# Performance work log

Measured on AMD Instinct MI355X. Metric: run time of the kernel, lower is better.

The kernel has to match this reference:

```python
import jax, jax.numpy as jnp
import numpy as np

NUM_CLASSES = 20
NUM_ANCHORS = 3
STRIDES = (8, 16, 32)
FMP = (320, 160, 80)
TOPK = 100
CONF_THRESH = 0.01
NMS_THRESH = 0.5
ANCHOR_SIZE = np.array([[12, 16], [19, 36], [40, 28], [36, 75], [76, 55], [72, 146],
                        [142, 110], [192, 243], [459, 401]], dtype=np.float32).reshape(3, NUM_ANCHORS, 2)


def make_anchors(level):
    h = w = FMP[level]
    ys, xs = jnp.meshgrid(jnp.arange(h, dtype=jnp.float32), jnp.arange(w, dtype=jnp.float32), indexing='ij')
    xy = jnp.stack([xs, ys], axis=-1).reshape(-1, 1, 2) + 0.5            # [HW,1,2] grid centers
    xy = jnp.broadcast_to(xy, (h * w, NUM_ANCHORS, 2))
    wh = jnp.broadcast_to(jnp.asarray(ANCHOR_SIZE[level]), (h * w, NUM_ANCHORS, 2))
    return jnp.concatenate([xy, wh], axis=-1).reshape(-1, 4)             # [HW*A, 4]


def level_topk(obj, cls, reg, level):
    C = NUM_CLASSES
    # [1, ch, H, W] -> [H*W*A, ch_per_anchor], matching permute(1,2,0).view(-1, .)
    obj = obj[0].transpose(1, 2, 0).reshape(-1, 1)
    cls = cls[0].transpose(1, 2, 0).reshape(-1, C)
    reg = reg[0].transpose(1, 2, 0).reshape(-1, 4)
    anchors = make_anchors(level)
    # decode: ctr = (sigmoid(txy)*3 - 1.5 + grid) * stride ; wh = exp(twh) * anchor_wh
    ctr = (jax.nn.sigmoid(reg[:, :2]) * 3.0 - 1.5 + anchors[:, :2]) * STRIDES[level]
    wh = jnp.exp(reg[:, 2:]) * anchors[:, 2:]
    boxes = jnp.concatenate([ctr - 0.5 * wh, ctr + 0.5 * wh], axis=-1)   # [N, 4] xyxy
    scores = (jax.nn.sigmoid(obj) * jax.nn.sigmoid(cls)).reshape(-1)     # [N*C]
    top_s, top_i = jax.lax.top_k(scores, TOPK)
    anchor_idx = top_i // C
    labels = top_i % C
    return top_s, labels, boxes[anchor_idx], top_s > CONF_THRESH


def nms_fixed(boxes, scores, labels, valid):
    # class-aware greedy NMS on a fixed candidate set; suppressed entries get score 0 / keep False
    K = scores.shape[0]
    order = jnp.argsort(-scores)
    b, s, l, v = boxes[order], scores[order], labels[order], valid[order]
    areas = (b[:, 2] - b[:, 0]) * (b[:, 3] - b[:, 1])
    xx1 = jnp.maximum(b[:, None, 0], b[None, :, 0])
    yy1 = jnp.maximum(b[:, None, 1], b[None, :, 1])
    xx2 = jnp.minimum(b[:, None, 2], b[None, :, 2])
    yy2 = jnp.minimum(b[:, None, 3], b[None, :, 3])
    inter = jnp.maximum(1e-10, xx2 - xx1) * jnp.maximum(1e-10, yy2 - yy1)
    iou = inter / (areas[:, None] + areas[None, :] - inter)
    sup_mat = (iou > NMS_THRESH) & (l[:, None] == l[None, :])            # per-class suppression
    idx = jnp.arange(K)

    def body(i, state):
        suppressed, keep = state
        is_kept = jnp.logical_and(jnp.logical_not(suppressed[i]), v[i])
        keep = keep.at[i].set(is_kept)
        suppressed = suppressed | (is_kept & sup_mat[i] & (idx > i))
        return suppressed, keep

    _, keep = jax.lax.fori_loop(0, K, body, (jnp.zeros(K, bool), jnp.zeros(K, bool)))
    return b, s * keep.astype(s.dtype), l, keep


def setup_inputs() -> dict:
    key = jax.random.key(0)
    ks = jax.random.split(key, 9)
    shapes = {
        'obj0': (1, NUM_ANCHORS, 320, 320), 'cls0': (1, NUM_ANCHORS * NUM_CLASSES, 320, 320), 'reg0': (1, NUM_ANCHORS * 4, 320, 320),
        'obj1': (1, NUM_ANCHORS, 160, 160), 'cls1': (1, NUM_ANCHORS * NUM_CLASSES, 160, 160), 'reg1': (1, NUM_ANCHORS * 4, 160, 160),
        'obj2': (1, NUM_ANCHORS, 80, 80), 'cls2': (1, NUM_ANCHORS * NUM_CLASSES, 80, 80), 'reg2': (1, NUM_ANCHORS * 4, 80, 80),
    }
    return {name: jax.random.normal(k, shp, dtype=jnp.float32)
            for k, (name, shp) in zip(ks, shapes.items())}


def reference(obj0, cls0, reg0, obj1, cls1, reg1, obj2, cls2, reg2):
    levels = [(obj0, cls0, reg0), (obj1, cls1, reg1), (obj2, cls2, reg2)]
    parts = [level_topk(o, c, r, i) for i, (o, c, r) in enumerate(levels)]
    scores = jnp.concatenate([p[0] for p in parts])
    labels = jnp.concatenate([p[1] for p in parts])
    boxes = jnp.concatenate([p[2] for p in parts])
    valid = jnp.concatenate([p[3] for p in parts])
    return nms_fixed(boxes, scores, labels, valid)  # (bboxes[300,4], scores[300], labels[300], keep[300])
```

## Files before the change

### kernel.cpp

```cpp
#include <hip/hip_runtime.h>
#include <stdint.h>

typedef unsigned int u32;
typedef unsigned long long u64;

#define TOPK 100
#define CAP 4096
#define NB 512
#define BINBASE 32000u
#define KAB_BLOCKS 788

__device__ const float ANC[3][3][2] = {
  {{12.f,16.f},{19.f,36.f},{40.f,28.f}},
  {{36.f,75.f},{76.f,55.f},{72.f,146.f}},
  {{142.f,110.f},{192.f,243.f},{459.f,401.f}}
};

__device__ __forceinline__ float sigmoidf_(float x) {
  if (x >= 0.f) return 1.f / (1.f + expf(-x));
  float e = expf(x);
  return e / (1.f + e);
}

__device__ __forceinline__ float fcomp2(const float2& v, int q) {
  return q ? v.y : v.x;
}

__global__ __launch_bounds__(256) void kA_scan(
    const float* __restrict__ obj0, const float* __restrict__ cls0,
    const float* __restrict__ obj1, const float* __restrict__ cls1,
    const float* __restrict__ obj2, const float* __restrict__ cls2,
    u32* __restrict__ hist, float* __restrict__ amax)
{
  __shared__ u32 h[NB];
  int tid = threadIdx.x;
  h[tid] = 0; h[tid + 256] = 0;
  __syncthreads();

  int b = blockIdx.x;
  const float *obj, *cls; int P, L, abase; u32 task;
  if (b < 600)      { L=0; obj=obj0; cls=cls0; P=102400; abase=0;      task=(u32)(b*256+tid); }
  else if (b < 750) { L=1; obj=obj1; cls=cls1; P=25600;  abase=307200; task=(u32)((b-600)*256+tid); }
  else              { L=2; obj=obj2; cls=cls2; P=6400;   abase=384000; task=(u32)((b-750)*256+tid); }
  int tpa = P >> 1;
  bool valid = task < (u32)(3*tpa);

  if (valid) {
    int a = (int)(task / (u32)tpa), rem = (int)(task % (u32)tpa);
    int p0 = rem * 2;
    float2 o2 = *(const float2*)(obj + a*P + p0);
    const float* cp = cls + (size_t)(a*20)*P + p0;
    float2 cv[20];
    #pragma unroll
    for (int k = 0; k < 20; ++k) cv[k] = *(const float2*)(cp + (size_t)k*P);
    float2 cm = cv[0];
    #pragma unroll
    for (int k = 1; k < 20; ++k) {
      cm.x = fmaxf(cm.x, cv[k].x); cm.y = fmaxf(cm.y, cv[k].y);
    }
    float2 am2;
    am2.x = sigmoidf_(o2.x) * sigmoidf_(cm.x);
    am2.y = sigmoidf_(o2.y) * sigmoidf_(cm.y);
    *(float2*)(amax + abase + a*P + p0) = am2;
    #pragma unroll
    for (int q = 0; q < 2; ++q) {
      u32 bt = __float_as_uint(fcomp2(am2, q));
      if (bt >= (BINBASE << 15)) {
        u32 bin = (bt >> 15) - BINBASE;
        if (bin < NB) atomicAdd(&h[bin], 1u);
      }
    }
  }
  __syncthreads();
  if (h[tid])       atomicAdd(&hist[L*NB + tid],       h[tid]);
  if (h[tid + 256]) atomicAdd(&hist[L*NB + tid + 256], h[tid + 256]);
}

__global__ __launch_bounds__(256) void kB_collect(
    const float* __restrict__ obj0, const float* __restrict__ cls0,
    const float* __restrict__ obj1, const float* __restrict__ cls1,
    const float* __restrict__ obj2, const float* __restrict__ cls2,
    const float* __restrict__ amax, const u32* __restrict__ hist,
    u32* __restrict__ cnt, u64* __restrict__ cand)
{
  __shared__ u32 s[NB];
  __shared__ u32 sThr;
  int tid = threadIdx.x;
  int b = blockIdx.x;
  const float *obj, *cls; int P, L, abase; u32 task;
  if (b < 600)      { L=0; obj=obj0; cls=cls0; P=102400; abase=0;      task=(u32)(b*256+tid); }
  else if (b < 750) { L=1; obj=obj1; cls=cls1; P=25600;  abase=307200; task=(u32)((b-600)*256+tid); }
  else              { L=2; obj=obj2; cls=cls2; P=6400;   abase=384000; task=(u32)((b-750)*256+tid); }
  int tpa = P >> 1;
  bool valid = task < (u32)(3*tpa);

  s[tid] = hist[L*NB + tid]; s[tid + 256] = hist[L*NB + tid + 256];
  __syncthreads();
  for (int off = 1; off < NB; off <<= 1) {
    u32 v0 = s[tid]       + ((tid + off < NB)       ? s[tid + off]       : 0u);
    u32 v1 = s[tid + 256] + ((tid + 256 + off < NB) ? s[tid + 256 + off] : 0u);
    __syncthreads();
    s[tid] = v0; s[tid + 256] = v1;
    __syncthreads();
  }
  if (tid == 0 && s[0] < TOPK) sThr = BINBASE << 15;
  {
    int i0 = tid, i1 = tid + 256;
    u32 a0 = s[i0], n0 = (i0 + 1 < NB) ? s[i0 + 1] : 0u;
    if (a0 >= TOPK && n0 < TOPK) sThr = (BINBASE + (u32)i0) << 15;
    u32 a1 = s[i1], n1 = (i1 + 1 < NB) ? s[i1 + 1] : 0u;
    if (a1 >= TOPK && n1 < TOPK) sThr = (BINBASE + (u32)i1) << 15;
  }
  __syncthreads();
  u32 thr = sThr;

  if (valid) {
    int a = (int)(task / (u32)tpa), rem = (int)(task % (u32)tpa);
    int p0 = rem * 2;
    float2 am2 = *(const float2*)(amax + abase + a*P + p0);
    bool any = (__float_as_uint(am2.x) >= thr) | (__float_as_uint(am2.y) >= thr);
    if (any) {
      float2 o2 = *(const float2*)(obj + a*P + p0);
      const float* cp = cls + (size_t)(a*20)*P + p0;
      float2 cv[20];
      #pragma unroll
      for (int k = 0; k < 20; ++k) cv[k] = *(const float2*)(cp + (size_t)k*P);
      #pragma unroll
      for (int q = 0; q < 2; ++q) {
        if (__float_as_uint(fcomp2(am2, q)) >= thr) {
          float so = sigmoidf_(fcomp2(o2, q));
          int p = p0 + q;
          #pragma unroll
          for (int k = 0; k < 20; ++k) {
            float sc = so * sigmoidf_(fcomp2(cv[k], q));
            u32 bits = __float_as_uint(sc);
            if (bits >= thr) {
              u32 pos = atomicAdd(&cnt[L], 1u);
              u32 idx = (u32)(p*60 + a*20 + k);
              if (pos < CAP) cand[L*CAP + pos] = ((u64)bits << 32) | (u64)(0x00FFFFFFu - idx);
            }
          }
        }
      }
    }
  }
}

__global__ __launch_bounds__(1024) void kC_select_nms(
    const float* __restrict__ reg0, const float* __restrict__ reg1, const float* __restrict__ reg2,
    const u64* __restrict__ cand, const u32* __restrict__ cnt,
    float* __restrict__ out)
{
  extern __shared__ uint8_t smem[];
  u64*    mat   = (u64*)(smem);
  float4* ibox4 = (float4*)(smem + 12000);
  float2* iml2  = (float2*)(smem + 16800);
  float*  x1s   = (float*)(smem + 19200);
  float*  y1s   = (float*)(smem + 20400);
  float*  x2s   = (float*)(smem + 21600);
  float*  y2s   = (float*)(smem + 22800);
  float*  sc2   = (float*)(smem + 24000);
  int*    lb2   = (int*)(smem + 25200);
  int*    vd2   = (int*)(smem + 26400);
  u64*    rowAny= (u64*)(smem + 27600);
  u64*    km    = (u64*)(smem + 27648);
  float*  ars   = (float*)(smem + 27696);
  u64*    sel   = (u64*)(smem + 32800);
  float*  bxs   = (float*)(smem + 35200);
  float*  scs   = (float*)(smem + 40000);
  int*    lbs   = (int*)(smem + 41200);
  int*    vds   = (int*)(smem + 42400);

  int tid = threadIdx.x;
  if (tid < 300) sel[tid] = 0ull;
  __syncthreads();

  {
    int gL    = (tid >= 768) ? 2 : (tid >= 384) ? 1 : 0;
    int gbase = (gL == 2) ? 768 : (gL == 1) ? 384 : 0;
    int lt    = tid - gbase;
    int gsz   = (gL == 2) ? 256 : 384;

    u32 n = cnt[gL]; if (n > CAP) n = CAP;
    bool useLds = (n <= 496);
    u64* kc = mat + gL*500;
    const u64* cb = cand + gL*CAP;
    u32 n4 = (n + 3u) & ~3u;

    if (useLds) {
      for (u32 j = (u32)lt; j < n; j += gsz) kc[j] = cb[j];
      if (lt < 4 && n + (u32)lt < n4) kc[n + lt] = 0ull;
    }
    __syncthreads();

    if (useLds) {
      for (u32 j = (u32)lt; j < n; j += gsz) {
        u64 kk = kc[j]; int r = 0;
        for (u32 t = 0; t < n4; t += 4) {
          u64 k0 = kc[t], k1 = kc[t+1], k2 = kc[t+2], k3 = kc[t+3];
          r += (k0 > kk) ? 1 : 0; r += (k1 > kk) ? 1 : 0;
          r += (k2 > kk) ? 1 : 0; r += (k3 > kk) ? 1 : 0;
        }
        if (r < TOPK) sel[gL*TOPK + r] = kk;
      }
    } else {
      u32 nn = n & ~3u;
      for (u32 j = (u32)lt; j < n; j += gsz) {
        u64 kk = cb[j]; int r = 0;
        for (u32 t = 0; t < nn; t += 4) {
          r += (cb[t]   > kk) ? 1 : 0; r += (cb[t+1] > kk) ? 1 : 0;
          r += (cb[t+2] > kk) ? 1 : 0; r += (cb[t+3] > kk) ? 1 : 0;
        }
        for (u32 t = nn; t < n; ++t) r += (cb[t] > kk) ? 1 : 0;
        if (r < TOPK) sel[gL*TOPK + r] = kk;
      }
    }
  }
  __syncthreads();

  if (tid < 300) {
    int Lq = tid / TOPK;
    const float* reg; int Pq, W, stride;
    if (Lq == 0)      { reg = reg0; Pq = 102400; W = 320; stride = 8; }
    else if (Lq == 1) { reg = reg1; Pq = 25600;  W = 160; stride = 16; }
    else              { reg = reg2; Pq = 6400;   W = 80;  stride = 32; }
    u64 key = sel[tid];
    if (key == 0) {
      scs[tid] = 0.f; lbs[tid] = 0; vds[tid] = 0;
      bxs[tid*4+0] = bxs[tid*4+1] = bxs[tid*4+2] = bxs[tid*4+3] = 0.f;
    } else {
      float score = __uint_as_float((u32)(key >> 32));
      u32 i = 0x00FFFFFFu - (u32)(key & 0xFFFFFFFFull);
      int c = (int)(i % 60u), p = (int)(i / 60u);
      int aa = c / 20, k = c % 20;
      int x = p % W, y = p / W;
      float tx = reg[(aa*4+0)*Pq + p], ty = reg[(aa*4+1)*Pq + p];
      float tw = reg[(aa*4+2)*Pq + p], th = reg[(aa*4+3)*Pq + p];
      float cx = (sigmoidf_(tx)*3.f - 1.5f + (float)x + 0.5f) * (float)stride;
      float cy = (sigmoidf_(ty)*3.f - 1.5f + (float)y + 0.5f) * (float)stride;
      float bw = expf(tw) * ANC[Lq][aa][0];
      float bh = expf(th) * ANC[Lq][aa][1];
      scs[tid] = score; lbs[tid] = k; vds[tid] = (score > 0.01f) ? 1 : 0;
      bxs[tid*4+0] = cx - 0.5f*bw; bxs[tid*4+1] = cy - 0.5f*bh;
      bxs[tid*4+2] = cx + 0.5f*bw; bxs[tid*4+3] = cy + 0.5f*bh;
    }
  }
  __syncthreads();

  if (tid < 300) {
    int Lm = tid / TOPK, rr = tid % TOPK;
    u64 kk = sel[tid];
    int rank = rr;
    #pragma unroll
    for (int Lo = 0; Lo < 3; ++Lo) {
      if (Lo == Lm) continue;
      const u64* arr = sel + Lo*TOPK;
      bool ge = (Lo < Lm);
      int lo = 0;
      #pragma unroll
      for (int st = 64; st > 0; st >>= 1) {
        int nxt = lo + st;
        if (nxt <= TOPK) {
          u64 v = arr[nxt - 1];
          bool pred = ge ? (v >= kk) : (v > kk);
          if (pred) lo = nxt;
        }
      }
      rank += lo;
    }
    float x1 = bxs[tid*4+0], y1 = bxs[tid*4+1], x2 = bxs[tid*4+2], y2 = bxs[tid*4+3];
    float ar = (x2 - x1) * (y2 - y1);
    ibox4[rank] = make_float4(x1, y1, x2, y2);
    iml2[rank]  = make_float2(ar, (float)lbs[tid]);
    x1s[rank] = x1; y1s[rank] = y1; x2s[rank] = x2; y2s[rank] = y2; ars[rank] = ar;
    sc2[rank] = scs[tid]; lb2[rank] = lbs[tid]; vd2[rank] = vds[tid];
  }
  __syncthreads();

  {
    int wave = tid >> 6, lane = tid & 63;
    if (wave < 15) {
      int w = (wave >= 10) ? 4 : (wave >= 6) ? 3 : (wave >= 3) ? 2 : (wave >= 1) ? 1 : 0;
      int ns = w + 1;
      int stripe = wave - ((w*(w+1)) >> 1);
      int j = w*64 + lane;
      bool jv = j < 300;
      float jx1=0.f, jy1=0.f, jx2=0.f, jy2=0.f, jar=0.f; float jlb=-1.f;
      if (jv) { jx1=x1s[j]; jy1=y1s[j]; jx2=x2s[j]; jy2=y2s[j]; jar=ars[j]; jlb=(float)lb2[j]; }
      int ilim = (w+1)*64; if (ilim > 300) ilim = 300;
      #pragma unroll 2
      for (int i = stripe; i < ilim; i += ns) {
        float4 B = ibox4[i];
        float2 M = iml2[i];
        float xx1 = fmaxf(B.x, jx1), yy1 = fmaxf(B.y, jy1);
        float xx2 = fminf(B.z, jx2), yy2 = fminf(B.w, jy2);
        float inter = fmaxf(1e-10f, xx2-xx1) * fmaxf(1e-10f, yy2-yy1);
        float iou = inter / (M.x + jar - inter);
        bool pred = jv && (iou > 0.5f) && (M.y == jlb);
        u64 m = __ballot(pred);
        if (lane == 0) mat[i*5 + w] = m;
      }
    }
  }
  __syncthreads();

  {
    bool flag = false;
    if (tid < 300) {
      int c = tid >> 6, bq = tid & 63;
      u64 acc = mat[tid*5 + c] & ((bq == 63) ? 0ull : (~0ull << (bq + 1)));
      for (int w = c + 1; w < 5; ++w) acc |= mat[tid*5 + w];
      flag = (acc != 0ull);
    }
    u64 bal = __ballot(flag);
    if ((tid & 63) == 0 && (tid >> 6) < 5) rowAny[tid >> 6] = bal;
  }
  __syncthreads();

  if (tid < 64) {
    int lane = tid;
    u64 vm[5];
    #pragma unroll
    for (int c = 0; c < 5; ++c) {
      int j = c*64 + lane;
      vm[c] = __ballot((j < 300) && (vd2[j] != 0));
    }
    u64 ra[5];
    #pragma unroll
    for (int c = 0; c < 5; ++c) ra[c] = rowAny[c];
    u64 S[5] = {0,0,0,0,0};
    #pragma unroll
    for (int c = 0; c < 5; ++c) {
      u64 kbits = 0;
      int lim = (c == 4) ? 44 : 64;
      for (int t = 0; t < lim; ++t) {
        u64 kept = ((~(S[c] >> t)) & (vm[c] >> t)) & 1ull;
        kbits |= kept << t;
        if (kept & ((ra[c] >> t) & 1ull)) {
          int i = c*64 + t;
          #pragma unroll
          for (int w = 0; w < 5; ++w)
            if (w >= c) S[w] |= mat[i*5 + w];
        }
      }
      if (lane == 0) km[c] = kbits;
    }
  }
  __syncthreads();

  if (tid < 300) {
    float kf = (float)((km[tid >> 6] >> (tid & 63)) & 1ull);
    float4 bq = ibox4[tid];
    out[tid*4+0] = bq.x; out[tid*4+1] = bq.y;
    out[tid*4+2] = bq.z; out[tid*4+3] = bq.w;
    out[1200+tid] = sc2[tid] * kf;
    out[1500+tid] = (float)lb2[tid];
    out[1800+tid] = kf;
  }
}

extern "C" void kernel_launch(void* const* d_in, const int* in_sizes, int n_in,
                              void* d_out, int out_size, void* d_ws, size_t ws_size,
                              hipStream_t stream) {
  const float* obj0 = (const float*)d_in[0];
  const float* cls0 = (const float*)d_in[1];
  const float* reg0 = (const float*)d_in[2];
  const float* obj1 = (const float*)d_in[3];
  const float* cls1 = (const float*)d_in[4];
  const float* reg1 = (const float*)d_in[5];
  const float* obj2 = (const float*)d_in[6];
  const float* cls2 = (const float*)d_in[7];
  const float* reg2 = (const float*)d_in[8];
  float* out = (float*)d_out;

  uint8_t* ws = (uint8_t*)d_ws;
  u32*   hist = (u32*)(ws + 0);
  u32*   cnt  = (u32*)(ws + 6144);
  u64*   cand = (u64*)(ws + 8192);
  float* amax = (float*)(ws + 106496);

  (void)hipMemsetAsync(ws, 0, 6160, stream);

  kA_scan<<<dim3(KAB_BLOCKS), dim3(256), 0, stream>>>(
      obj0, cls0, obj1, cls1, obj2, cls2, hist, amax);
  kB_collect<<<dim3(KAB_BLOCKS), dim3(256), 0, stream>>>(
      obj0, cls0, obj1, cls1, obj2, cls2, amax, hist, cnt, cand);
  kC_select_nms<<<dim3(1), dim3(1024), 43600, stream>>>(reg0, reg1, reg2, cand, cnt, out);
}
```

Measured before the change: 155.7 us.

## Split NMS IoU matrix across five blocks with global-memory barrier

The single-block select+NMS kernel now launches 5 blocks. Each block redundantly runs candidate selection, then computes one 64-column stripe of the IoU suppression matrix. Blocks 1-4 write their stripes to global memory and signal an atomic counter, and block 0 spins on it before loading them into LDS. The goal is to spread the IoU matrix work across more compute units, at the cost of duplicated selection work, a spin-wait, and a global round trip.

```diff
diff --git a/kernel.cpp b/kernel.cpp
--- a/kernel.cpp
+++ b/kernel.cpp
@@ -146,9 +146,10 @@
   }
 }
 
-__global__ __launch_bounds__(1024) void kC_select_nms(
+__global__ __launch_bounds__(1024) void kT_select_nms(
     const float* __restrict__ reg0, const float* __restrict__ reg1, const float* __restrict__ reg2,
     const u64* __restrict__ cand, const u32* __restrict__ cnt,
+    u64* __restrict__ matg, u32* __restrict__ bar,
     float* __restrict__ out)
 {
   extern __shared__ uint8_t smem[];
@@ -172,6 +173,7 @@
   int*    vds   = (int*)(smem + 42400);
 
   int tid = threadIdx.x;
+  int b = blockIdx.x;
   if (tid < 300) sel[tid] = 0ull;
   __syncthreads();
 
@@ -278,29 +280,45 @@
   __syncthreads();
 
   {
+    int w = (b == 0) ? 4 : (b - 1);
     int wave = tid >> 6, lane = tid & 63;
-    if (wave < 15) {
-      int w = (wave >= 10) ? 4 : (wave >= 6) ? 3 : (wave >= 3) ? 2 : (wave >= 1) ? 1 : 0;
-      int ns = w + 1;
-      int stripe = wave - ((w*(w+1)) >> 1);
-      int j = w*64 + lane;
-      bool jv = j < 300;
-      float jx1=0.f, jy1=0.f, jx2=0.f, jy2=0.f, jar=0.f; float jlb=-1.f;
-      if (jv) { jx1=x1s[j]; jy1=y1s[j]; jx2=x2s[j]; jy2=y2s[j]; jar=ars[j]; jlb=(float)lb2[j]; }
-      int ilim = (w+1)*64; if (ilim > 300) ilim = 300;
-      #pragma unroll 2
-      for (int i = stripe; i < ilim; i += ns) {
-        float4 B = ibox4[i];
-        float2 M = iml2[i];
-        float xx1 = fmaxf(B.x, jx1), yy1 = fmaxf(B.y, jy1);
-        float xx2 = fminf(B.z, jx2), yy2 = fminf(B.w, jy2);
-        float inter = fmaxf(1e-10f, xx2-xx1) * fmaxf(1e-10f, yy2-yy1);
-        float iou = inter / (M.x + jar - inter);
-        bool pred = jv && (iou > 0.5f) && (M.y == jlb);
-        u64 m = __ballot(pred);
-        if (lane == 0) mat[i*5 + w] = m;
-      }
-    }
+    int j = w*64 + lane;
+    bool jv = j < 300;
+    float jx1=0.f, jy1=0.f, jx2=0.f, jy2=0.f, jar=0.f; float jlb=-1.f;
+    if (jv) { jx1=x1s[j]; jy1=y1s[j]; jx2=x2s[j]; jy2=y2s[j]; jar=ars[j]; jlb=(float)lb2[j]; }
+    int ilim = (w+1)*64; if (ilim > 300) ilim = 300;
+    for (int i = wave; i < ilim; i += 16) {
+      float4 B = ibox4[i];
+      float2 M = iml2[i];
+      float xx1 = fmaxf(B.x, jx1), yy1 = fmaxf(B.y, jy1);
+      float xx2 = fminf(B.z, jx2), yy2 = fminf(B.w, jy2);
+      float inter = fmaxf(1e-10f, xx2-xx1) * fmaxf(1e-10f, yy2-yy1);
+      float iou = inter / (M.x + jar - inter);
+      bool pred = jv && (iou > 0.5f) && (M.y == jlb);
+      u64 m = __ballot(pred);
+      if (lane == 0) {
+        if (b == 0) mat[i*5 + 4] = m;
+        else __hip_atomic_store(&matg[i*5 + w], m, __ATOMIC_RELAXED, __HIP_MEMORY_SCOPE_AGENT);
+      }
+    }
+  }
+  __syncthreads();
+
+  if (b != 0) {
+    if (tid == 0)
+      __hip_atomic_fetch_add(bar, 1u, __ATOMIC_RELEASE, __HIP_MEMORY_SCOPE_AGENT);
+    return;
+  }
+
+  if (tid == 0) {
+    while (__hip_atomic_load(bar, __ATOMIC_ACQUIRE, __HIP_MEMORY_SCOPE_AGENT) < 4u)
+      __builtin_amdgcn_s_sleep(1);
+  }
+  __syncthreads();
+  for (int idx = tid; idx < 1200; idx += 1024) {
+    int w2 = idx / 300, i = idx % 300;
+    if (i < (w2+1)*64)
+      mat[i*5 + w2] = __hip_atomic_load(&matg[i*5 + w2], __ATOMIC_RELAXED, __HIP_MEMORY_SCOPE_AGENT);
   }
   __syncthreads();
 
@@ -376,8 +394,10 @@
   uint8_t* ws = (uint8_t*)d_ws;
   u32*   hist = (u32*)(ws + 0);
   u32*   cnt  = (u32*)(ws + 6144);
+  u32*   bar  = (u32*)(ws + 6156);
   u64*   cand = (u64*)(ws + 8192);
-  float* amax = (float*)(ws + 106496);
+  u64*   matg = (u64*)(ws + 106496);
+  float* amax = (float*)(ws + 118496);
 
   (void)hipMemsetAsync(ws, 0, 6160, stream);
 
@@ -385,5 +405,6 @@
       obj0, cls0, obj1, cls1, obj2, cls2, hist, amax);
   kB_collect<<<dim3(KAB_BLOCKS), dim3(256), 0, stream>>>(
       obj0, cls0, obj1, cls1, obj2, cls2, amax, hist, cnt, cand);
-  kC_select_nms<<<dim3(1), dim3(1024), 43600, stream>>>(reg0, reg1, reg2, cand, cnt, out);
-}
+  kT_select_nms<<<dim3(5), dim3(1024), 43600, stream>>>(
+      reg0, reg1, reg2, cand, cnt, matg, bar, out);
+}
```

Measured after the change: 146.2 us. 6.1% less time.
